# Kernel optimization log

Measured on AMD Instinct MI355X. Metric: run time of the kernel, lower is better.

Reference implementation:

```python
import jax, jax.numpy as jnp
import numpy as np

Q_DIM = 1024
K_DIM = 1024
HID = 128
EPS = 1e-5


def setup_inputs() -> dict:
    key = jax.random.key(0)
    ks = jax.random.split(key, 12)
    B, Tq, Tk = 2, 512, 512
    s_q = 1.0 / np.sqrt(Q_DIM)
    s_k = 1.0 / np.sqrt(K_DIM)
    s_h3 = 1.0 / np.sqrt(3 * HID)
    s_h = 1.0 / np.sqrt(HID)
    return {
        "Q": jax.random.normal(ks[0], (B, Tq, Q_DIM), jnp.float32),
        "K": jax.random.normal(ks[1], (B, Tk, K_DIM), jnp.float32),
        "Wq": jax.random.uniform(ks[2], (Q_DIM, HID), jnp.float32, -s_q, s_q),
        "Wk": jax.random.uniform(ks[3], (K_DIM, HID), jnp.float32, -s_k, s_k),
        "ln_g": jnp.ones((3 * HID,), jnp.float32),
        "ln_b": jnp.zeros((3 * HID,), jnp.float32),
        "Wu": jax.random.uniform(ks[4], (3 * HID, HID), jnp.float32, -s_h3, s_h3),
        "bu": jax.random.uniform(ks[5], (HID,), jnp.float32, -s_h3, s_h3),
        "Wv": jax.random.uniform(ks[6], (3 * HID, HID), jnp.float32, -s_h3, s_h3),
        "bv": jax.random.uniform(ks[7], (HID,), jnp.float32, -s_h3, s_h3),
        "Wo": jax.random.uniform(ks[8], (HID, 1), jnp.float32, -s_h, s_h),
        "bo": jax.random.uniform(ks[9], (1,), jnp.float32, -s_h, s_h),
    }


def reference(Q, K, Wq, Wk, ln_g, ln_b, Wu, bu, Wv, bv, Wo, bo):
    B, Tq, _ = Q.shape
    Tk = K.shape[1]
    q = jnp.einsum("bqd,dh->bqh", Q, Wq)              # (B,Tq,H)
    k = jnp.einsum("bkd,dh->bkh", K, Wk)              # (B,Tk,H)
    q_exp = jnp.broadcast_to(q[:, :, None, :], (B, Tq, Tk, HID))
    k_exp = jnp.broadcast_to(k[:, None, :, :], (B, Tq, Tk, HID))
    x = jnp.concatenate([q_exp, k_exp, q_exp * k_exp], axis=-1)  # (B,Tq,Tk,3H)
    mu = jnp.mean(x, axis=-1, keepdims=True)
    var = jnp.mean(jnp.square(x - mu), axis=-1, keepdims=True)
    x = (x - mu) * jax.lax.rsqrt(var + EPS) * ln_g + ln_b
    u = jnp.einsum("bqkc,ch->bqkh", x, Wu) + bu
    v = jnp.einsum("bqkc,ch->bqkh", x, Wv) + bv
    z = u * jax.nn.gelu(v, approximate=False)
    return (jnp.einsum("bqkh,ho->bqko", z, Wo) + bo)[..., 0]  # (B,Tq,Tk)
```

## Files before the change

kernel.cpp:

```cpp
#include <hip/hip_runtime.h>
#include <hip/hip_bf16.h>
#include <math.h>


#define EPSLN 1e-5f

#define WS_QP   0
#define WS_KP   131072
#define WS_PU   262144
#define WS_PV   393216
#define WS_RU   524288
#define WS_RV   655360
#define WS_SQ   786432
#define WS_QQ   787456
#define WS_SK   788480
#define WS_KK   789504
#define WS_GUS  790528
#define WS_GVS  790656
#define WS_CU   790784
#define WS_CV   790912
#define WS_WTU  791040
#define WS_WTV  815616
#define WS_WQT  840192
#define WS_WKT  905728

typedef __attribute__((ext_vector_type(8))) short short8;
typedef __attribute__((ext_vector_type(4))) float f32x4;

__device__ inline unsigned short f2bf(float x) {
    unsigned u = __builtin_bit_cast(unsigned, x);
    unsigned r = u + 0x7fffu + ((u >> 16) & 1u);
    return (unsigned short)(r >> 16);
}
__device__ inline float b2f_lo(unsigned v) { return __builtin_bit_cast(float, v << 16); }
__device__ inline float b2f_hi(unsigned v) { return __builtin_bit_cast(float, v & 0xffff0000u); }
__device__ inline unsigned pack_bf2(float a, float b) {
    __hip_bfloat162 h = __float22bfloat162_rn(make_float2(a, b));
    unsigned r;
    __builtin_memcpy(&r, &h, 4);
    return r;
}
__device__ inline void store8(unsigned short* p, const unsigned short* v) {
    short8 s;
    #pragma unroll
    for (int e = 0; e < 8; ++e) s[e] = (short)v[e];
    *(short8*)p = s;
}
#define GELU_C1 2.3022035f
#define GELU_C2 0.1029431f
__device__ inline float fast_gelu(float v) {
    float ex = __builtin_amdgcn_exp2f(v * fmaf(v * v, GELU_C2, GELU_C1));
    float r  = __builtin_amdgcn_rcpf(ex + 1.f);
    return v - v * r;
}

__global__ __launch_bounds__(256, 2)
void k_prep(const float* __restrict__ Wu, const float* __restrict__ bu,
            const float* __restrict__ Wv, const float* __restrict__ bv,
            const float* __restrict__ g, const float* __restrict__ bln,
            const float* __restrict__ Wo,
            const float* __restrict__ Wq, const float* __restrict__ Wk,
            float* __restrict__ ws) {
    int task = blockIdx.x, t = threadIdx.x;
    if (task < 2) {
        bool isV = task != 0;
        const float* W  = isV ? Wv : Wu;
        const float* bb = isV ? bv : bu;
        float* gout = ws + (isV ? WS_GVS : WS_GUS);
        float* cout = ws + (isV ? WS_CV : WS_CU);
        __shared__ float rg[2][128], rc[2][128];
        int tl = t & 127, g2 = t >> 7;
        float gu = 0.f, cu = 0.f;
        #pragma unroll 4
        for (int c = g2 * 192; c < g2 * 192 + 192; ++c) {
            float wv_ = W[c * 128 + tl];
            gu += g[c] * wv_;
            cu += bln[c] * wv_;
        }
        rg[g2][tl] = gu; rc[g2][tl] = cu;
        __syncthreads();
        if (t < 128) gout[t] = rg[0][t] + rg[1][t];
        else { int h = t - 128; cout[h] = rc[0][h] + rc[1][h] + bb[h]; }
    } else if (task < 8) {
        int tt = task - 2;
        bool isV = tt >= 3;
        int seg = tt % 3;
        const float* W = isV ? Wv : Wu;
        unsigned short* wt = (unsigned short*)(ws + (isV ? WS_WTV : WS_WTU));
        __shared__ unsigned short tile[128 * 130];
        for (int it = 0; it < 64; ++it) {
            int idx = t + 256 * it;
            int c = idx >> 7, h = idx & 127;
            float s = g[seg * 128 + c] * (isV ? 1.f : Wo[h]);
            tile[c * 130 + h] = f2bf(s * W[(seg * 128 + c) * 128 + h]);
        }
        __syncthreads();
        int h = t >> 1, c0 = (t & 1) * 64;
        for (int cc = 0; cc < 64; cc += 8) {
            unsigned short v[8];
            #pragma unroll
            for (int e = 0; e < 8; ++e) v[e] = tile[(c0 + cc + e) * 130 + h];
            store8(&wt[h * 384 + seg * 128 + c0 + cc], v);
        }
    } else {
        int tt = task - 8;
        const float* W = (tt >> 3) ? Wk : Wq;
        unsigned short* wt = (unsigned short*)(ws + ((tt >> 3) ? WS_WKT : WS_WQT));
        int seg = tt & 7;
        __shared__ unsigned short tile[128 * 130];
        for (int it = 0; it < 64; ++it) {
            int idx = t + 256 * it;
            int c = idx >> 7, h = idx & 127;
            tile[c * 130 + h] = f2bf(W[(size_t)(seg * 128 + c) * 128 + h]);
        }
        __syncthreads();
        int h = t >> 1, c0 = (t & 1) * 64;
        for (int cc = 0; cc < 64; cc += 8) {
            unsigned short v[8];
            #pragma unroll
            for (int e = 0; e < 8; ++e) v[e] = tile[(c0 + cc + e) * 130 + h];
            store8(&wt[h * 1024 + seg * 128 + c0 + cc], v);
        }
    }
}

#define XST 1028
#define QST 132
__global__ __launch_bounds__(256, 2)
void k_proj(const float* __restrict__ Q, const float* __restrict__ K,
            float* __restrict__ ws) {
    int blk = blockIdx.x, t = threadIdx.x;
    bool isK = blk >= 128;
    int r0 = (blk & 127) * 8;
    const float* src = isK ? K : Q;
    const unsigned short* wtin = (const unsigned short*)(ws + (isK ? WS_WKT : WS_WQT));
    float* dst = ws + (isK ? WS_KP : WS_QP);
    int L = t & 63, w = t >> 6;
    int col = L & 15, quad = L >> 4;

    __shared__ unsigned short XLb[16 * XST];
    __shared__ unsigned short qpL[16 * QST];
    __shared__ float sp1[16][4], sp2[16][4];

    {
        int srow = t >> 5;
        int c0 = (t & 31) * 4;
        const float* sp = src + (size_t)(r0 + srow) * 1024;
        #pragma unroll
        for (int g8 = 0; g8 < 8; ++g8) {
            float4 xv = *(const float4*)(sp + g8 * 128 + c0);
            unsigned* xp = (unsigned*)&XLb[srow * XST + g8 * 128 + c0];
            xp[0] = pack_bf2(xv.x, xv.y);
            xp[1] = pack_bf2(xv.z, xv.w);
        }
    }
    __syncthreads();

    f32x4 acc[2];
    acc[0] = (f32x4){0.f, 0.f, 0.f, 0.f};
    acc[1] = (f32x4){0.f, 0.f, 0.f, 0.f};
    #pragma unroll 4
    for (int ks = 0; ks < 32; ++ks) {
        short8 a = *(const short8*)&XLb[col * XST + ks * 32 + quad * 8];
        #pragma unroll
        for (int nt2 = 0; nt2 < 2; ++nt2) {
            int h = w * 32 + nt2 * 16 + col;
            short8 b = *(const short8*)&wtin[(size_t)h * 1024 + ks * 32 + quad * 8];
            acc[nt2] = __builtin_amdgcn_mfma_f32_16x16x32_bf16(a, b, acc[nt2], 0, 0, 0);
        }
    }

    #pragma unroll
    for (int r = 0; r < 4; ++r) {
        int row = quad * 4 + r;
        float s1 = acc[0][r] + acc[1][r];
        float s2 = acc[0][r] * acc[0][r] + acc[1][r] * acc[1][r];
        #pragma unroll
        for (int d = 1; d < 16; d <<= 1) { s1 += __shfl_xor(s1, d); s2 += __shfl_xor(s2, d); }
        if (col == 0) { sp1[row][w] = s1; sp2[row][w] = s2; }
        #pragma unroll
        for (int nt2 = 0; nt2 < 2; ++nt2) {
            int h = w * 32 + nt2 * 16 + col;
            qpL[row * QST + h] = f2bf(acc[nt2][r]);
            if (row < 8) dst[(size_t)(r0 + row) * 128 + h] = acc[nt2][r];
        }
    }
    __syncthreads();
    if (t < 8) {
        ws[(isK ? WS_SK : WS_SQ) + r0 + t] = (sp1[t][0] + sp1[t][1]) + (sp1[t][2] + sp1[t][3]);
        ws[(isK ? WS_KK : WS_QQ) + r0 + t] = (sp2[t][0] + sp2[t][1]) + (sp2[t][2] + sp2[t][3]);
    }

    int uv = w & 1, nhf = w >> 1;
    const unsigned short* wt = (const unsigned short*)(ws + (uv ? WS_WTV : WS_WTU));
    int cb0 = isK ? 128 : 0;
    f32x4 pacc[4];
    #pragma unroll
    for (int nt = 0; nt < 4; ++nt) pacc[nt] = (f32x4){0.f, 0.f, 0.f, 0.f};
    #pragma unroll
    for (int ks = 0; ks < 4; ++ks) {
        short8 a = *(const short8*)&qpL[col * QST + ks * 32 + quad * 8];
        #pragma unroll
        for (int nt = 0; nt < 4; ++nt) {
            int h = nhf * 64 + nt * 16 + col;
            short8 b = *(const short8*)&wt[h * 384 + cb0 + ks * 32 + quad * 8];
            pacc[nt] = __builtin_amdgcn_mfma_f32_16x16x32_bf16(a, b, pacc[nt], 0, 0, 0);
        }
    }
    float* PO = ws + (uv ? (isK ? WS_RV : WS_PV) : (isK ? WS_RU : WS_PU));
    #pragma unroll
    for (int nt = 0; nt < 4; ++nt)
        #pragma unroll
        for (int r = 0; r < 4; ++r) {
            int row = quad * 4 + r;
            if (row < 8)
                PO[(size_t)(r0 + row) * 128 + nhf * 64 + nt * 16 + col] = pacc[nt][r];
        }
}

#define ASTR 152
#define RSTR 132
#define REDS 132
#define PST  136
__global__ __launch_bounds__(512, 4)
void k_main(const float* __restrict__ ws, float* __restrict__ out,
            const float* __restrict__ Wo, const float* __restrict__ bo) {
    int blk = blockIdx.x;
    int jt = blk & 15, ig = (blk >> 4) & 31, b = blk >> 9;
    int t = threadIdx.x;
    int L = t & 63, w = t >> 6;
    int col = L & 15, quad = L >> 4;
    int krow0 = b * 512 + jt * 32;
    int jj = t >> 4, cb = (t & 15) * 8;
    int h = w * 16 + col;

    __shared__ __align__(16) char smem[47616];
    unsigned short* Alds = (unsigned short*)smem;
    float*          red2 = (float*)(smem + 9728);
    unsigned short* QL   = (unsigned short*)smem;
    unsigned short* Q2L  = (unsigned short*)(smem + 4352);
    unsigned short* KL   = (unsigned short*)(smem + 8704);
    unsigned short* K2L  = (unsigned short*)(smem + 17408);
    unsigned*       ruvL = (unsigned*)(smem + 26624);
    float*          rsL2 = (float*)(smem + 43520);

    int bi0 = b * 512 + ig * 16;

    float kreg[8];
    {
        const float* kp = ws + WS_KP + (size_t)(krow0 + jj) * 128 + cb;
        #pragma unroll
        for (int e = 0; e < 8; ++e) kreg[e] = kp[e];
        const float* rup = ws + WS_RU + (size_t)(krow0 + jj) * 128 + cb;
        const float* rvp = ws + WS_RV + (size_t)(krow0 + jj) * 128 + cb;
        unsigned pk[8];
        #pragma unroll
        for (int e = 0; e < 8; ++e) pk[e] = pack_bf2(rup[e], rvp[e]);
        unsigned* rr = &ruvL[jj * RSTR + cb];
        *(uint4*)&rr[0] = *(uint4*)&pk[0];
        *(uint4*)&rr[4] = *(uint4*)&pk[4];
        unsigned kk4[4], k2[4];
        #pragma unroll
        for (int e = 0; e < 4; ++e) {
            kk4[e] = pack_bf2(kreg[e * 2], kreg[e * 2 + 1]);
            k2[e]  = pack_bf2(kreg[e * 2] * kreg[e * 2], kreg[e * 2 + 1] * kreg[e * 2 + 1]);
        }
        *(uint4*)&KL[jj * PST + cb]  = *(uint4*)&kk4[0];
        *(uint4*)&K2L[jj * PST + cb] = *(uint4*)&k2[0];
    }
    {
        int row = t >> 5, c0 = (t & 31) * 4;
        float4 qv = *(const float4*)(ws + WS_QP + (size_t)(bi0 + row) * 128 + c0);
        unsigned q01 = pack_bf2(qv.x, qv.y), q23 = pack_bf2(qv.z, qv.w);
        unsigned s01 = pack_bf2(qv.x * qv.x, qv.y * qv.y);
        unsigned s23 = pack_bf2(qv.z * qv.z, qv.w * qv.w);
        uint2 qp = make_uint2(q01, q23), sp = make_uint2(s01, s23);
        *(uint2*)&QL[row * PST + c0]  = qp;
        *(uint2*)&Q2L[row * PST + c0] = sp;
    }

    short8 w3f[2][4];
    {
        const unsigned short* wtu = (const unsigned short*)(ws + WS_WTU);
        const unsigned short* wtv = (const unsigned short*)(ws + WS_WTV);
        #pragma unroll
        for (int ks = 0; ks < 4; ++ks) {
            w3f[0][ks] = *(const short8*)&wtu[h * 384 + 256 + ks * 32 + quad * 8];
            w3f[1][ks] = *(const short8*)&wtv[h * 384 + 256 + ks * 32 + quad * 8];
        }
    }
    float wo  = Wo[h];
    float gusv = ws[WS_GUS + h] * wo;
    float cuv  = ws[WS_CU + h] * wo;
    float gvsv = ws[WS_GVS + h];
    float cvv  = ws[WS_CV + h];
    float bo0 = bo[0];

    int bi = bi0;
    float4 qA = *(const float4*)(ws + WS_QP + (size_t)bi * 128 + cb);
    float4 qB = *(const float4*)(ws + WS_QP + (size_t)bi * 128 + cb + 4);
    float puv = ws[WS_PU + (size_t)bi * 128 + h];
    float pvv = ws[WS_PV + (size_t)bi * 128 + h];
    __syncthreads();

    if (w < 2) {
        int j = w * 16 + col;
        f32x4 d1a = (f32x4){0.f, 0.f, 0.f, 0.f};
        f32x4 d2a = (f32x4){0.f, 0.f, 0.f, 0.f};
        #pragma unroll
        for (int ks = 0; ks < 4; ++ks) {
            short8 aq  = *(const short8*)&QL[col * PST + ks * 32 + quad * 8];
            short8 bk  = *(const short8*)&KL[j * PST + ks * 32 + quad * 8];
            d1a = __builtin_amdgcn_mfma_f32_16x16x32_bf16(aq, bk, d1a, 0, 0, 0);
            short8 aq2 = *(const short8*)&Q2L[col * PST + ks * 32 + quad * 8];
            short8 bk2 = *(const short8*)&K2L[j * PST + ks * 32 + quad * 8];
            d2a = __builtin_amdgcn_mfma_f32_16x16x32_bf16(aq2, bk2, d2a, 0, 0, 0);
        }
        float skj = ws[WS_SK + krow0 + j];
        float kkj = ws[WS_KK + krow0 + j];
        #pragma unroll
        for (int r = 0; r < 4; ++r) {
            int i = quad * 4 + r;
            float mu = (ws[WS_SQ + bi0 + i] + skj + d1a[r]) * (1.0f / 384.0f);
            float e2 = (ws[WS_QQ + bi0 + i] + kkj + d2a[r]) * (1.0f / 384.0f);
            float rs = rsqrtf(e2 - mu * mu + EPSLN);
            *(float2*)&rsL2[(i * 32 + j) * 2] = make_float2(rs, rs * mu);
        }
    }
    __syncthreads();

    #pragma unroll 1
    for (int ii = 0; ii < 16; ++ii) {
        {
            unsigned pk[4];
            float x0 = kreg[0] * qA.x, x1 = kreg[1] * qA.y;
            float x2 = kreg[2] * qA.z, x3 = kreg[3] * qA.w;
            float y0 = kreg[4] * qB.x, y1 = kreg[5] * qB.y;
            float y2 = kreg[6] * qB.z, y3 = kreg[7] * qB.w;
            pk[0] = pack_bf2(x0, x1); pk[1] = pack_bf2(x2, x3);
            pk[2] = pack_bf2(y0, y1); pk[3] = pack_bf2(y2, y3);
            unsigned* arow = (unsigned*)Alds + jj * (ASTR / 2) + cb / 2;
            *(uint4*)&arow[0] = *(uint4*)&pk[0];
        }
        int bin = bi0 + ((ii + 1) & 15);
        float4 qA2 = *(const float4*)(ws + WS_QP + (size_t)bin * 128 + cb);
        float4 qB2 = *(const float4*)(ws + WS_QP + (size_t)bin * 128 + cb + 4);
        float pu2 = ws[WS_PU + (size_t)bin * 128 + h];
        float pv2 = ws[WS_PV + (size_t)bin * 128 + h];
        __syncthreads();
        f32x4 acc[2][2];
        #pragma unroll
        for (int mt = 0; mt < 2; ++mt)
            #pragma unroll
            for (int uv = 0; uv < 2; ++uv) acc[mt][uv] = (f32x4){0.f, 0.f, 0.f, 0.f};
        #pragma unroll
        for (int ks = 0; ks < 4; ++ks) {
            short8 a0 = *(const short8*)&Alds[col * ASTR + ks * 32 + quad * 8];
            short8 a1 = *(const short8*)&Alds[(col + 16) * ASTR + ks * 32 + quad * 8];
            acc[0][0] = __builtin_amdgcn_mfma_f32_16x16x32_bf16(a0, w3f[0][ks], acc[0][0], 0, 0, 0);
            acc[0][1] = __builtin_amdgcn_mfma_f32_16x16x32_bf16(a0, w3f[1][ks], acc[0][1], 0, 0, 0);
            acc[1][0] = __builtin_amdgcn_mfma_f32_16x16x32_bf16(a1, w3f[0][ks], acc[1][0], 0, 0, 0);
            acc[1][1] = __builtin_amdgcn_mfma_f32_16x16x32_bf16(a1, w3f[1][ks], acc[1][1], 0, 0, 0);
        }
        #pragma unroll
        for (int mt = 0; mt < 2; ++mt) {
            #pragma unroll
            for (int r = 0; r < 4; ++r) {
                int jl = mt * 16 + quad * 4 + r;
                float2 rp = *(const float2*)&rsL2[(ii * 32 + jl) * 2];
                float rs = rp.x, rsmu = rp.y;
                unsigned pr = ruvL[jl * RSTR + h];
                float su  = acc[mt][0][r] + puv + b2f_lo(pr);
                float u   = fmaf(rs, su, fmaf(-rsmu, gusv, cuv));
                float sv_ = acc[mt][1][r] + pvv + b2f_hi(pr);
                float v   = fmaf(rs, sv_, fmaf(-rsmu, gvsv, cvv));
                red2[jl * REDS + w * 16 + col] = u * fast_gelu(v);
            }
        }
        __syncthreads();
        if (t < 128) {
            const float4* rr = (const float4*)&red2[(t >> 2) * REDS];
            int k = t & 3;
            float s = 0.f;
            #pragma unroll
            for (int c4 = 0; c4 < 8; ++c4) {
                float4 x = rr[k + c4 * 4];
                s += (x.x + x.y) + (x.z + x.w);
            }
            s += __shfl_xor(s, 1);
            s += __shfl_xor(s, 2);
            if (k == 0)
                out[(size_t)bi * 512 + jt * 32 + (t >> 2)] = s + bo0;
        }
        qA = qA2; qB = qB2; puv = pu2; pvv = pv2; bi = bin;
    }
}

extern "C" void kernel_launch(void* const* d_in, const int* in_sizes, int n_in,
                              void* d_out, int out_size, void* d_ws, size_t ws_size,
                              hipStream_t stream) {
    const float* Q   = (const float*)d_in[0];
    const float* K   = (const float*)d_in[1];
    const float* Wq  = (const float*)d_in[2];
    const float* Wk  = (const float*)d_in[3];
    const float* g   = (const float*)d_in[4];
    const float* bln = (const float*)d_in[5];
    const float* Wu  = (const float*)d_in[6];
    const float* bu  = (const float*)d_in[7];
    const float* Wv  = (const float*)d_in[8];
    const float* bv  = (const float*)d_in[9];
    const float* Wo  = (const float*)d_in[10];
    const float* bo  = (const float*)d_in[11];
    float* ws  = (float*)d_ws;
    float* out = (float*)d_out;

    hipLaunchKernelGGL(k_prep, dim3(24), dim3(256), 0, stream, Wu, bu, Wv, bv, g, bln, Wo, Wq, Wk, ws);
    hipLaunchKernelGGL(k_proj, dim3(256), dim3(256), 0, stream, Q, K, ws);
    hipLaunchKernelGGL(k_main, dim3(1024), dim3(512), 0, stream, ws, out, Wo, bo);
}
```

Before: 192.7 us.

## Keep per-key bias pairs in registers, trim LDS, relax barriers and widen reduction

The packed per-key bias pairs (RU/RV) move from shared memory into per-thread registers, which shrinks the shared allocation and may allow more resident blocks. Next-row prefetch loads are issued at the top of the loop and the loop is unrolled by two. The q-side bias is folded into the MFMA accumulator initialisation, and the rs/mu values are read as float4. __syncthreads becomes an inline s_waitcnt lgkmcnt(0) plus s_barrier, and the final row reduction uses 256 threads instead of 128. The costs are higher register pressure and a hand-written barrier that only waits on LDS/scalar counters, not on outstanding vector memory ops.

```diff
diff --git a/kernel.cpp b/kernel.cpp
--- a/kernel.cpp
+++ b/kernel.cpp
@@ -53,6 +53,7 @@
     float r  = __builtin_amdgcn_rcpf(ex + 1.f);
     return v - v * r;
 }
+#define BAR_LDS() asm volatile("s_waitcnt lgkmcnt(0)\n\ts_barrier" ::: "memory")
 
 __global__ __launch_bounds__(256, 2)
 void k_prep(const float* __restrict__ Wu, const float* __restrict__ bu,
@@ -219,7 +220,6 @@
 }
 
 #define ASTR 152
-#define RSTR 132
 #define REDS 132
 #define PST  136
 __global__ __launch_bounds__(512, 4)
@@ -234,15 +234,14 @@
     int jj = t >> 4, cb = (t & 15) * 8;
     int h = w * 16 + col;
 
-    __shared__ __align__(16) char smem[47616];
+    __shared__ __align__(16) char smem[30720];
     unsigned short* Alds = (unsigned short*)smem;
     float*          red2 = (float*)(smem + 9728);
     unsigned short* QL   = (unsigned short*)smem;
     unsigned short* Q2L  = (unsigned short*)(smem + 4352);
     unsigned short* KL   = (unsigned short*)(smem + 8704);
     unsigned short* K2L  = (unsigned short*)(smem + 17408);
-    unsigned*       ruvL = (unsigned*)(smem + 26624);
-    float*          rsL2 = (float*)(smem + 43520);
+    float*          rsL2 = (float*)(smem + 26624);
 
     int bi0 = b * 512 + ig * 16;
 
@@ -251,14 +250,6 @@
         const float* kp = ws + WS_KP + (size_t)(krow0 + jj) * 128 + cb;
         #pragma unroll
         for (int e = 0; e < 8; ++e) kreg[e] = kp[e];
-        const float* rup = ws + WS_RU + (size_t)(krow0 + jj) * 128 + cb;
-        const float* rvp = ws + WS_RV + (size_t)(krow0 + jj) * 128 + cb;
-        unsigned pk[8];
-        #pragma unroll
-        for (int e = 0; e < 8; ++e) pk[e] = pack_bf2(rup[e], rvp[e]);
-        unsigned* rr = &ruvL[jj * RSTR + cb];
-        *(uint4*)&rr[0] = *(uint4*)&pk[0];
-        *(uint4*)&rr[4] = *(uint4*)&pk[4];
         unsigned kk4[4], k2[4];
         #pragma unroll
         for (int e = 0; e < 4; ++e) {
@@ -278,6 +269,16 @@
         *(uint2*)&QL[row * PST + c0]  = qp;
         *(uint2*)&Q2L[row * PST + c0] = sp;
     }
+    unsigned prR[8];
+    #pragma unroll
+    for (int mt = 0; mt < 2; ++mt)
+        #pragma unroll
+        for (int r = 0; r < 4; ++r) {
+            int jl = mt * 16 + quad * 4 + r;
+            float ru = ws[WS_RU + (size_t)(krow0 + jl) * 128 + h];
+            float rv = ws[WS_RV + (size_t)(krow0 + jl) * 128 + h];
+            prR[mt * 4 + r] = pack_bf2(ru, rv);
+        }
 
     short8 w3f[2][4];
     {
@@ -329,8 +330,13 @@
     }
     __syncthreads();
 
-    #pragma unroll 1
+    #pragma unroll 2
     for (int ii = 0; ii < 16; ++ii) {
+        int bin = bi0 + ((ii + 1) & 15);
+        float4 qA2 = *(const float4*)(ws + WS_QP + (size_t)bin * 128 + cb);
+        float4 qB2 = *(const float4*)(ws + WS_QP + (size_t)bin * 128 + cb + 4);
+        float pu2 = ws[WS_PU + (size_t)bin * 128 + h];
+        float pv2 = ws[WS_PV + (size_t)bin * 128 + h];
         {
             unsigned pk[4];
             float x0 = kreg[0] * qA.x, x1 = kreg[1] * qA.y;
@@ -342,17 +348,13 @@
             unsigned* arow = (unsigned*)Alds + jj * (ASTR / 2) + cb / 2;
             *(uint4*)&arow[0] = *(uint4*)&pk[0];
         }
-        int bin = bi0 + ((ii + 1) & 15);
-        float4 qA2 = *(const float4*)(ws + WS_QP + (size_t)bin * 128 + cb);
-        float4 qB2 = *(const float4*)(ws + WS_QP + (size_t)bin * 128 + cb + 4);
-        float pu2 = ws[WS_PU + (size_t)bin * 128 + h];
-        float pv2 = ws[WS_PV + (size_t)bin * 128 + h];
-        __syncthreads();
+        BAR_LDS();
         f32x4 acc[2][2];
         #pragma unroll
-        for (int mt = 0; mt < 2; ++mt)
-            #pragma unroll
-            for (int uv = 0; uv < 2; ++uv) acc[mt][uv] = (f32x4){0.f, 0.f, 0.f, 0.f};
+        for (int mt = 0; mt < 2; ++mt) {
+            acc[mt][0] = (f32x4){puv, puv, puv, puv};
+            acc[mt][1] = (f32x4){pvv, pvv, pvv, pvv};
+        }
         #pragma unroll
         for (int ks = 0; ks < 4; ++ks) {
             short8 a0 = *(const short8*)&Alds[col * ASTR + ks * 32 + quad * 8];
@@ -364,33 +366,36 @@
         }
         #pragma unroll
         for (int mt = 0; mt < 2; ++mt) {
+            float4 s0 = *(const float4*)&rsL2[(ii * 32 + mt * 16 + quad * 4) * 2];
+            float4 s1 = *(const float4*)&rsL2[(ii * 32 + mt * 16 + quad * 4) * 2 + 4];
             #pragma unroll
             for (int r = 0; r < 4; ++r) {
+                float rs   = r == 0 ? s0.x : r == 1 ? s0.z : r == 2 ? s1.x : s1.z;
+                float rsmu = r == 0 ? s0.y : r == 1 ? s0.w : r == 2 ? s1.y : s1.w;
                 int jl = mt * 16 + quad * 4 + r;
-                float2 rp = *(const float2*)&rsL2[(ii * 32 + jl) * 2];
-                float rs = rp.x, rsmu = rp.y;
-                unsigned pr = ruvL[jl * RSTR + h];
-                float su  = acc[mt][0][r] + puv + b2f_lo(pr);
+                unsigned pr = prR[mt * 4 + r];
+                float su  = acc[mt][0][r] + b2f_lo(pr);
                 float u   = fmaf(rs, su, fmaf(-rsmu, gusv, cuv));
-                float sv_ = acc[mt][1][r] + pvv + b2f_hi(pr);
+                float sv_ = acc[mt][1][r] + b2f_hi(pr);
                 float v   = fmaf(rs, sv_, fmaf(-rsmu, gvsv, cvv));
                 red2[jl * REDS + w * 16 + col] = u * fast_gelu(v);
             }
         }
-        __syncthreads();
-        if (t < 128) {
-            const float4* rr = (const float4*)&red2[(t >> 2) * REDS];
-            int k = t & 3;
+        BAR_LDS();
+        if (t < 256) {
+            const float4* rr = (const float4*)&red2[(t >> 3) * REDS];
+            int k = t & 7;
             float s = 0.f;
             #pragma unroll
-            for (int c4 = 0; c4 < 8; ++c4) {
-                float4 x = rr[k + c4 * 4];
+            for (int c4 = 0; c4 < 4; ++c4) {
+                float4 x = rr[k + c4 * 8];
                 s += (x.x + x.y) + (x.z + x.w);
             }
             s += __shfl_xor(s, 1);
             s += __shfl_xor(s, 2);
+            s += __shfl_xor(s, 4);
             if (k == 0)
-                out[(size_t)bi * 512 + jt * 32 + (t >> 2)] = s + bo0;
+                out[(size_t)bi * 512 + jt * 32 + (t >> 3)] = s + bo0;
         }
         qA = qA2; qB = qB2; puv = pu2; pvv = pv2; bi = bin;
     }
```

Result: faster. 183.4 us (-4.8%).
